# Performance work log

Measured on AMD Instinct MI355X. Metric: run time of the kernel, lower is better.

## Reference

```python
import jax, jax.numpy as jnp
import numpy as np

B, K, D = 8, 2048, 1024

def setup_inputs() -> dict:
    key = jax.random.key(0)
    k1, k2 = jax.random.split(key)
    x = jax.random.normal(k1, (B, K, D), dtype=jnp.float32)
    W = jax.random.normal(k2, (K, K), dtype=jnp.float32) * 0.02  # dt_proj weight [out=K, in=K]
    b = jnp.zeros((K,), dtype=jnp.float32)                        # dt_proj bias
    return {"x": x, "W": W, "b": b}

def _scan_combine(c1, c2):
    # compose affine maps s -> a*s + u; (a1,u1) then (a2,u2)
    a1, u1 = c1
    a2, u2 = c2
    return (a2 * a1, a2 * u1 + u2)

def reference(x, W, b):
    # lam[b,t,d] = sigmoid( sum_k x[b,k,d] * W[t,k] + b[t] )
    # (dt_proj is a Linear over the TIME axis after permute(0,2,1))
    lam = jax.nn.sigmoid(jnp.einsum('bkd,tk->btd', x, W) + b[None, :, None])
    # s_t = lam_t * s_{t-1} + (1 - lam_t) * x_t, s_0 = 0  -> associative scan over time
    _, ys = jax.lax.associative_scan(_scan_combine, (lam, (1.0 - lam) * x), axis=1)
    return ys
```

## Files before the change

kernel.cpp:

```cpp
#include <hip/hip_runtime.h>
#include <hip/hip_bf16.h>
#include <stdint.h>

#define B_ 8
#define K_ 2048
#define D_ 1024
#define NC 32
#define TC (K_ / NC)

typedef float v4f __attribute__((ext_vector_type(4)));
typedef short v8s __attribute__((ext_vector_type(8)));

__device__ __forceinline__ unsigned short f2bf(float f) {
    __hip_bfloat16 h = __float2bfloat16(f);
    return *reinterpret_cast<unsigned short*>(&h);
}

__device__ __forceinline__ void async_ld16(const void* g, void* l) {
    __builtin_amdgcn_global_load_lds(
        (__attribute__((address_space(1))) void*)(void*)g,
        (__attribute__((address_space(3))) void*)l,
        16, 0, 0);
}

__global__ void conv_w(const float* __restrict__ W, unsigned short* __restrict__ Wb) {
    int i = (blockIdx.x * 256 + threadIdx.x) * 4;
    float4 v = *(const float4*)(W + i);
    ushort4 o;
    o.x = f2bf(v.x); o.y = f2bf(v.y); o.z = f2bf(v.z); o.w = f2bf(v.w);
    *(ushort4*)(Wb + i) = o;
}

__global__ void conv_x_t(const float* __restrict__ x, unsigned short* __restrict__ xT) {
    const int k0 = blockIdx.x * 64, d0 = blockIdx.y * 64, bb = blockIdx.z;
    __shared__ unsigned short tile[64][68];
    const int tid = threadIdx.x;
    const int tx = tid & 15, ty = tid >> 4;
    const float* xp = x + (size_t)bb * K_ * D_;
#pragma unroll
    for (int r = 0; r < 4; r++) {
        int row = ty + r * 16;
        float4 v = *(const float4*)(xp + (size_t)(k0 + row) * D_ + d0 + tx * 4);
        tile[row][tx * 4 + 0] = f2bf(v.x);
        tile[row][tx * 4 + 1] = f2bf(v.y);
        tile[row][tx * 4 + 2] = f2bf(v.z);
        tile[row][tx * 4 + 3] = f2bf(v.w);
    }
    __syncthreads();
    unsigned short* op = xT + (size_t)bb * D_ * K_;
#pragma unroll
    for (int r = 0; r < 4; r++) {
        int dcol = ty + r * 16;
        ushort4 u;
        u.x = tile[tx * 4 + 0][dcol];
        u.y = tile[tx * 4 + 1][dcol];
        u.z = tile[tx * 4 + 2][dcol];
        u.w = tile[tx * 4 + 3][dcol];
        *(ushort4*)(op + (size_t)(d0 + dcol) * K_ + k0 + tx * 4) = u;
    }
}

__launch_bounds__(256)
__global__ void gemm_sig(const unsigned short* __restrict__ Wb,
                         const unsigned short* __restrict__ xT,
                         const float* __restrict__ bias,
                         float* __restrict__ lam) {
    const int tM = blockIdx.x, tN = blockIdx.y, bb = blockIdx.z;
    __shared__ unsigned short As[128 * 32];
    __shared__ unsigned short Bs[128 * 32];
    const int tid = threadIdx.x;
    const int w = tid >> 6;
    const int lane = tid & 63;
    const int wm = w >> 1, wn = w & 1;
    const int quad = lane >> 4;
    const int l16 = lane & 15;

    v4f acc[4][4];
#pragma unroll
    for (int i = 0; i < 4; i++)
#pragma unroll
        for (int j = 0; j < 4; j++) acc[i][j] = (v4f)0.f;

    const unsigned short* Ag = Wb + (size_t)(tM * 128) * K_;
    const unsigned short* Bg = xT + (size_t)bb * D_ * K_ + (size_t)(tN * 128) * K_;

    const int srow = lane >> 2;
    const int schunk = (((lane & 3) ^ ((lane >> 3) & 3)) * 8);
    const int sw8 = (quad ^ ((l16 >> 1) & 3)) * 8;

    for (int k0 = 0; k0 < K_; k0 += 32) {
#pragma unroll
        for (int q = 0; q < 2; q++) {
            int rb = (q * 4 + w) * 16;
            async_ld16(Ag + (size_t)(rb + srow) * K_ + k0 + schunk, As + rb * 32);
            async_ld16(Bg + (size_t)(rb + srow) * K_ + k0 + schunk, Bs + rb * 32);
        }
        __syncthreads();
        v8s af[4], bfr[4];
#pragma unroll
        for (int i = 0; i < 4; i++)
            af[i] = *(const v8s*)(As + (wm * 64 + i * 16 + l16) * 32 + sw8);
#pragma unroll
        for (int j = 0; j < 4; j++)
            bfr[j] = *(const v8s*)(Bs + (wn * 64 + j * 16 + l16) * 32 + sw8);
#pragma unroll
        for (int i = 0; i < 4; i++)
#pragma unroll
            for (int j = 0; j < 4; j++)
                acc[i][j] = __builtin_amdgcn_mfma_f32_16x16x32_bf16(af[i], bfr[j], acc[i][j], 0, 0, 0);
        __syncthreads();
    }

    float* out = lam + (size_t)bb * K_ * D_;
#pragma unroll
    for (int i = 0; i < 4; i++) {
        int rowb = tM * 128 + wm * 64 + i * 16 + quad * 4;
#pragma unroll
        for (int r = 0; r < 4; r++) {
            float bt = bias[rowb + r];
#pragma unroll
            for (int j = 0; j < 4; j++) {
                int col = tN * 128 + wn * 64 + j * 16 + l16;
                float v = acc[i][j][r] + bt;
                out[(size_t)(rowb + r) * D_ + col] = 1.f / (1.f + __expf(-v));
            }
        }
    }
}

__global__ void scan_pass1(const float* __restrict__ lam, const float* __restrict__ x,
                           float* __restrict__ Ac, float* __restrict__ Uc) {
    int id = blockIdx.x * 256 + threadIdx.x;
    int d = id & (D_ - 1);
    int c = (id >> 10) & (NC - 1);
    int bb = id >> 15;
    const float* lp = lam + (size_t)bb * K_ * D_ + (size_t)c * TC * D_ + d;
    const float* xp = x   + (size_t)bb * K_ * D_ + (size_t)c * TC * D_ + d;
    float A = 1.f, U = 0.f;
#pragma unroll 8
    for (int t = 0; t < TC; t++) {
        float l = lp[(size_t)t * D_];
        float xv = xp[(size_t)t * D_];
        A *= l;
        U = l * U + (1.f - l) * xv;
    }
    Ac[id] = A;
    Uc[id] = U;
}

__global__ void scan_pass2(const float* __restrict__ Ac, const float* __restrict__ Uc,
                           float* __restrict__ Sin) {
    int id = blockIdx.x * 256 + threadIdx.x;
    int d = id & (D_ - 1);
    int bb = id >> 10;
    float s = 0.f;
#pragma unroll
    for (int c = 0; c < NC; c++) {
        int idx = (bb * NC + c) * D_ + d;
        Sin[idx] = s;
        s = Ac[idx] * s + Uc[idx];
    }
}

__global__ void scan_pass3(const float* __restrict__ x, const float* __restrict__ Sin,
                           float* __restrict__ lamout) {
    int id = blockIdx.x * 256 + threadIdx.x;
    int d = id & (D_ - 1);
    int c = (id >> 10) & (NC - 1);
    int bb = id >> 15;
    float* lp = lamout + (size_t)bb * K_ * D_ + (size_t)c * TC * D_ + d;
    const float* xp = x + (size_t)bb * K_ * D_ + (size_t)c * TC * D_ + d;
    float s = Sin[id];
#pragma unroll 8
    for (int t = 0; t < TC; t++) {
        float l = lp[(size_t)t * D_];
        float xv = xp[(size_t)t * D_];
        s = l * s + (1.f - l) * xv;
        lp[(size_t)t * D_] = s;
    }
}

extern "C" void kernel_launch(void* const* d_in, const int* in_sizes, int n_in,
                              void* d_out, int out_size, void* d_ws, size_t ws_size,
                              hipStream_t stream) {
    const float* x    = (const float*)d_in[0];
    const float* W    = (const float*)d_in[1];
    const float* bias = (const float*)d_in[2];
    float* out = (float*)d_out;
    char* ws = (char*)d_ws;

    unsigned short* xT = (unsigned short*)ws;
    unsigned short* Wb = (unsigned short*)(ws + 33554432);
    float* Ac  = (float*)(ws + 33554432);
    float* Uc  = (float*)(ws + 33554432 + 1048576);
    float* Sin = (float*)(ws + 33554432 + 2097152);

    conv_w<<<dim3(K_ * K_ / 4 / 256), 256, 0, stream>>>(W, Wb);
    conv_x_t<<<dim3(K_ / 64, D_ / 64, B_), 256, 0, stream>>>(x, xT);
    gemm_sig<<<dim3(K_ / 128, D_ / 128, B_), 256, 0, stream>>>(Wb, xT, bias, out);
    scan_pass1<<<dim3(B_ * NC * D_ / 256), 256, 0, stream>>>(out, x, Ac, Uc);
    scan_pass2<<<dim3(B_ * D_ / 256), 256, 0, stream>>>(Ac, Uc, Sin);
    scan_pass3<<<dim3(B_ * NC * D_ / 256), 256, 0, stream>>>(x, Sin, out);
}
```

Before: 281.6 us.

## Double K-step per barrier in GEMM, drop LDS swizzle, vectorize scan passes to float2

The GEMM now loads two 32-wide K slices per iteration into two LDS buffers, so barriers are paid once per 64 K instead of once per 32. It also drops the XOR swizzle on LDS stores and reads, which can bring back bank conflicts on fragment reads. The scan passes 1 and 3 each thread two adjacent d columns with float2 loads and stores and launch half as many threads, which cuts parallelism during the latency-bound serial loops.

Result: no change. 277.3 us (-1.5%).

```diff
diff --git a/kernel.cpp b/kernel.cpp
--- a/kernel.cpp
+++ b/kernel.cpp
@@ -66,8 +66,8 @@
                          const float* __restrict__ bias,
                          float* __restrict__ lam) {
     const int tM = blockIdx.x, tN = blockIdx.y, bb = blockIdx.z;
-    __shared__ unsigned short As[128 * 32];
-    __shared__ unsigned short Bs[128 * 32];
+    __shared__ unsigned short As[2][128 * 32];
+    __shared__ unsigned short Bs[2][128 * 32];
     const int tid = threadIdx.x;
     const int w = tid >> 6;
     const int lane = tid & 63;
@@ -85,29 +85,34 @@
     const unsigned short* Bg = xT + (size_t)bb * D_ * K_ + (size_t)(tN * 128) * K_;
 
     const int srow = lane >> 2;
-    const int schunk = (((lane & 3) ^ ((lane >> 3) & 3)) * 8);
-    const int sw8 = (quad ^ ((l16 >> 1) & 3)) * 8;
-
-    for (int k0 = 0; k0 < K_; k0 += 32) {
-#pragma unroll
-        for (int q = 0; q < 2; q++) {
-            int rb = (q * 4 + w) * 16;
-            async_ld16(Ag + (size_t)(rb + srow) * K_ + k0 + schunk, As + rb * 32);
-            async_ld16(Bg + (size_t)(rb + srow) * K_ + k0 + schunk, Bs + rb * 32);
+    const int schunk = (lane & 3) * 8;
+
+    for (int k0 = 0; k0 < K_; k0 += 64) {
+#pragma unroll
+        for (int h = 0; h < 2; h++) {
+#pragma unroll
+            for (int q = 0; q < 2; q++) {
+                int rb = (q * 4 + w) * 16;
+                async_ld16(Ag + (size_t)(rb + srow) * K_ + k0 + h * 32 + schunk, &As[h][rb * 32]);
+                async_ld16(Bg + (size_t)(rb + srow) * K_ + k0 + h * 32 + schunk, &Bs[h][rb * 32]);
+            }
         }
         __syncthreads();
-        v8s af[4], bfr[4];
-#pragma unroll
-        for (int i = 0; i < 4; i++)
-            af[i] = *(const v8s*)(As + (wm * 64 + i * 16 + l16) * 32 + sw8);
-#pragma unroll
-        for (int j = 0; j < 4; j++)
-            bfr[j] = *(const v8s*)(Bs + (wn * 64 + j * 16 + l16) * 32 + sw8);
-#pragma unroll
-        for (int i = 0; i < 4; i++)
+#pragma unroll
+        for (int h = 0; h < 2; h++) {
+            v8s af[4], bfr[4];
+#pragma unroll
+            for (int i = 0; i < 4; i++)
+                af[i] = *(const v8s*)(&As[h][(wm * 64 + i * 16 + l16) * 32 + quad * 8]);
 #pragma unroll
             for (int j = 0; j < 4; j++)
-                acc[i][j] = __builtin_amdgcn_mfma_f32_16x16x32_bf16(af[i], bfr[j], acc[i][j], 0, 0, 0);
+                bfr[j] = *(const v8s*)(&Bs[h][(wn * 64 + j * 16 + l16) * 32 + quad * 8]);
+#pragma unroll
+            for (int i = 0; i < 4; i++)
+#pragma unroll
+                for (int j = 0; j < 4; j++)
+                    acc[i][j] = __builtin_amdgcn_mfma_f32_16x16x32_bf16(af[i], bfr[j], acc[i][j], 0, 0, 0);
+        }
         __syncthreads();
     }
 
@@ -131,21 +136,23 @@
 __global__ void scan_pass1(const float* __restrict__ lam, const float* __restrict__ x,
                            float* __restrict__ Ac, float* __restrict__ Uc) {
     int id = blockIdx.x * 256 + threadIdx.x;
-    int d = id & (D_ - 1);
-    int c = (id >> 10) & (NC - 1);
-    int bb = id >> 15;
-    const float* lp = lam + (size_t)bb * K_ * D_ + (size_t)c * TC * D_ + d;
-    const float* xp = x   + (size_t)bb * K_ * D_ + (size_t)c * TC * D_ + d;
-    float A = 1.f, U = 0.f;
+    int d2 = (id & 511) * 2;
+    int c = (id >> 9) & (NC - 1);
+    int bb = id >> 14;
+    const float* lp = lam + ((size_t)bb * K_ + (size_t)c * TC) * D_ + d2;
+    const float* xp = x   + ((size_t)bb * K_ + (size_t)c * TC) * D_ + d2;
+    float2 A = make_float2(1.f, 1.f), U = make_float2(0.f, 0.f);
 #pragma unroll 8
     for (int t = 0; t < TC; t++) {
-        float l = lp[(size_t)t * D_];
-        float xv = xp[(size_t)t * D_];
-        A *= l;
-        U = l * U + (1.f - l) * xv;
-    }
-    Ac[id] = A;
-    Uc[id] = U;
+        float2 l  = *(const float2*)(lp + (size_t)t * D_);
+        float2 xv = *(const float2*)(xp + (size_t)t * D_);
+        A.x *= l.x; A.y *= l.y;
+        U.x = l.x * U.x + (1.f - l.x) * xv.x;
+        U.y = l.y * U.y + (1.f - l.y) * xv.y;
+    }
+    size_t oi = ((size_t)bb * NC + c) * D_ + d2;
+    *(float2*)(Ac + oi) = A;
+    *(float2*)(Uc + oi) = U;
 }
 
 __global__ void scan_pass2(const float* __restrict__ Ac, const float* __restrict__ Uc,
@@ -165,18 +172,20 @@
 __global__ void scan_pass3(const float* __restrict__ x, const float* __restrict__ Sin,
                            float* __restrict__ lamout) {
     int id = blockIdx.x * 256 + threadIdx.x;
-    int d = id & (D_ - 1);
-    int c = (id >> 10) & (NC - 1);
-    int bb = id >> 15;
-    float* lp = lamout + (size_t)bb * K_ * D_ + (size_t)c * TC * D_ + d;
-    const float* xp = x + (size_t)bb * K_ * D_ + (size_t)c * TC * D_ + d;
-    float s = Sin[id];
+    int d2 = (id & 511) * 2;
+    int c = (id >> 9) & (NC - 1);
+    int bb = id >> 14;
+    float* lp = lamout + ((size_t)bb * K_ + (size_t)c * TC) * D_ + d2;
+    const float* xp = x + ((size_t)bb * K_ + (size_t)c * TC) * D_ + d2;
+    size_t si = ((size_t)bb * NC + c) * D_ + d2;
+    float2 s = *(const float2*)(Sin + si);
 #pragma unroll 8
     for (int t = 0; t < TC; t++) {
-        float l = lp[(size_t)t * D_];
-        float xv = xp[(size_t)t * D_];
-        s = l * s + (1.f - l) * xv;
-        lp[(size_t)t * D_] = s;
+        float2 l  = *(const float2*)(lp + (size_t)t * D_);
+        float2 xv = *(const float2*)(xp + (size_t)t * D_);
+        s.x = l.x * s.x + (1.f - l.x) * xv.x;
+        s.y = l.y * s.y + (1.f - l.y) * xv.y;
+        *(float2*)(lp + (size_t)t * D_) = s;
     }
 }
 
@@ -198,7 +207,7 @@
     conv_w<<<dim3(K_ * K_ / 4 / 256), 256, 0, stream>>>(W, Wb);
     conv_x_t<<<dim3(K_ / 64, D_ / 64, B_), 256, 0, stream>>>(x, xT);
     gemm_sig<<<dim3(K_ / 128, D_ / 128, B_), 256, 0, stream>>>(Wb, xT, bias, out);
-    scan_pass1<<<dim3(B_ * NC * D_ / 256), 256, 0, stream>>>(out, x, Ac, Uc);
+    scan_pass1<<<dim3(B_ * NC * D_ / 2 / 256), 256, 0, stream>>>(out, x, Ac, Uc);
     scan_pass2<<<dim3(B_ * D_ / 256), 256, 0, stream>>>(Ac, Uc, Sin);
-    scan_pass3<<<dim3(B_ * NC * D_ / 256), 256, 0, stream>>>(x, Sin, out);
-}
+    scan_pass3<<<dim3(B_ * NC * D_ / 2 / 256), 256, 0, stream>>>(x, Sin, out);
+}
```
